# Optimization experiments

Hardware: AMD Instinct MI355X
Metric: run time of the kernel (lower is better)

## Reference

```python
import jax, jax.numpy as jnp
import numpy as np

N, T = 4096, 1024
COND, PRED, PERIOD = 896, 56, 7


def setup_inputs() -> dict:
    key = jax.random.key(0)
    k1, k2 = jax.random.split(key)
    query = jax.random.normal(k1, (N, T), dtype=jnp.float32)
    # learned per-location params: [init_level, level_sm_logit, init_trend,
    #  trend_sm_logit, season_sm, period seasonality logits]
    params = 0.1 * jax.random.normal(k2, (N, 5 + PERIOD), dtype=jnp.float32)
    return {"query": query, "params": params}


def _forward(query, params):
    init_level = params[:, 0]                       # [N]
    level_sm = jax.nn.sigmoid(params[:, 1])         # [N]
    init_trend = params[:, 2]                       # [N]
    trend_sm = jax.nn.sigmoid(params[:, 3])         # [N]
    season_sm = params[:, 4]                        # NOTE: no sigmoid, matches original code
    init_seas = jax.nn.sigmoid(params[:, -PERIOD:])  # [N, PERIOD]

    def step(carry, y):
        prev_level, prev_trend, buf = carry          # buf: rolling window of last PERIOD seasonalities
        s_t = buf[:, 0]                              # seasonalities[t]
        pred = prev_level + prev_trend
        level = level_sm * y + (1.0 - level_sm) * pred
        diff = jnp.abs(level - prev_level)
        trend = trend_sm * (level - prev_level) + (1.0 - trend_sm) * prev_trend
        new_seas = season_sm * (y - pred) + (1.0 - season_sm) * s_t
        buf = jnp.concatenate([buf[:, 1:], new_seas[:, None]], axis=1)
        return (level, trend, buf), (level, trend, new_seas, diff)

    carry0 = (init_level, init_trend, init_seas)
    _, (levels, trends, new_seas_seq, diffs) = jax.lax.scan(step, carry0, query.T)
    levels = levels.T            # [N, T]
    trends = trends.T            # [N, T]
    new_seas_seq = new_seas_seq.T  # [N, T], == seasonalities[:, PERIOD:]
    level_diffs = diffs.T.mean(axis=1)  # [N]

    # full seasonality sequence: PERIOD initial values followed by T computed ones
    seas_full = jnp.concatenate([init_seas, new_seas_seq], axis=1)  # [N, PERIOD+T]

    sm = query - levels - new_seas_seq  # [N, T]

    horizon = jnp.arange(1, PRED + 1, dtype=levels.dtype)  # [PRED]
    last_levels = levels[:, COND - 1:, None]   # [N, W, 1], W = T-COND+1
    last_trends = trends[:, COND - 1:, None]
    pr = last_levels + last_trends * horizon   # [N, W, PRED]

    # cyclic seasonality forecast per window
    season_index = jnp.tile(jnp.arange(PERIOD), (PRED + PERIOD - 1) // PERIOD)[:PRED]
    starts = jnp.arange(COND, T + 1)           # [W]
    idx = starts[:, None] + season_index[None, :]  # [W, PRED]
    pr = pr + seas_full[:, idx]                # [N, W, PRED]

    return sm, pr, level_diffs


def reference(query, params):
    return _forward(query, params)
```

## Files before the change

### kernel.cpp

```cpp
#include <hip/hip_runtime.h>
#include <cmath>

#define NROWS 4096
#define TLEN  1024
#define RPB   8
#define LT0   895
#define ST0   889
#define LTN   129
#define STN   135
#define PRV4R 1806
#define PRV4B (RPB * PRV4R)

__device__ __forceinline__ float sigmoidf_(float x) {
    return 1.0f / (1.0f + expf(-x));
}

__device__ __forceinline__ float f4c(const float4& v, int k) {
    switch (k & 3) { case 0: return v.x; case 1: return v.y; case 2: return v.z; default: return v.w; }
}

__global__ __launch_bounds__(256, 2)
void es_fused(const float* __restrict__ query,
              const float* __restrict__ params,
              float* __restrict__ sm,
              float* __restrict__ diffs,
              float4* __restrict__ pr4)
{
    __shared__ float lds_P[RPB * 65];
    __shared__ float lds_start[RPB * 65];
    __shared__ float lds_q[RPB * 225];
    __shared__ float lds_dsum[RPB * 33];
    __shared__ float lds_par[RPB * 16];
    __shared__ float Ltl[RPB * 132];
    __shared__ float Ttl[RPB * 132];
    __shared__ float Stl[RPB * 136];

    const int tid = threadIdx.x;
    const int r = tid >> 5;
    const int k = tid & 31;
    const int n = blockIdx.x * RPB + r;

    const float* pp = params + (size_t)n * 12;
    const float a  = sigmoidf_(pp[1]);
    const float b  = sigmoidf_(pp[3]);
    const float c  = pp[4];
    const float ia = 1.0f - a, ib = 1.0f - b, ic = 1.0f - c;

    float4 yv[8];
    {
        const float4* qv = reinterpret_cast<const float4*>(query + (size_t)n * TLEN + k * 32);
        #pragma unroll
        for (int i = 0; i < 8; ++i) yv[i] = qv[i];
    }

    {
        float L = 0.0f, B = 0.0f;
        #pragma unroll
        for (int j = 0; j < 32; ++j) {
            const float yy = f4c(yv[j >> 2], j);
            const float pred  = L + B;
            const float level = fmaf(a, yy, ia * pred);
            const float trend = fmaf(b, level - L, ib * B);
            L = level; B = trend;
        }
        lds_P[r * 65 + 2 * k]     = L;
        lds_P[r * 65 + 2 * k + 1] = B;
    }
    if (k == 0) {
        float* par = &lds_par[r * 16];
        par[0] = pp[0];
        par[1] = pp[2];
        par[2] = ia;
        par[3] = -(a * b);
        par[4] = ib + b * ia;
        par[5] = ic;
        #pragma unroll
        for (int l = 0; l < 7; ++l) par[6 + l] = sigmoidf_(pp[5 + l]);
    }
    __syncthreads();

    if (tid < 8) {
        const float* par = &lds_par[tid * 16];
        float m00 = par[2], m01 = par[2], m10 = par[3], m11 = par[4];
        #pragma unroll
        for (int s = 0; s < 5; ++s) {
            const float t00 = m00 * m00 + m01 * m10;
            const float t01 = m00 * m01 + m01 * m11;
            const float t10 = m10 * m00 + m11 * m10;
            const float t11 = m10 * m01 + m11 * m11;
            m00 = t00; m01 = t01; m10 = t10; m11 = t11;
        }
        float P0[32], P1[32];
        #pragma unroll
        for (int kk = 0; kk < 32; ++kk) {
            P0[kk] = lds_P[tid * 65 + 2 * kk];
            P1[kk] = lds_P[tid * 65 + 2 * kk + 1];
        }
        float s0 = par[0], s1 = par[1];
        #pragma unroll
        for (int kk = 0; kk < 32; ++kk) {
            lds_start[tid * 65 + 2 * kk]     = s0;
            lds_start[tid * 65 + 2 * kk + 1] = s1;
            const float t0 = m00 * s0 + m01 * s1 + P0[kk];
            const float t1 = m10 * s0 + m11 * s1 + P1[kk];
            s0 = t0; s1 = t1;
        }
    }
    __syncthreads();

    const float st0 = lds_start[r * 65 + 2 * k];
    const float st1 = lds_start[r * 65 + 2 * k + 1];

    {
        float L = st0, B = st1, dsum = 0.0f;
        float q[7] = {0,0,0,0,0,0,0};
        #pragma unroll
        for (int j = 0; j < 32; ++j) {
            const float yy = f4c(yv[j >> 2], j);
            const float pred  = L + B;
            const float level = fmaf(a, yy, ia * pred);
            const float d     = level - L;
            dsum += fabsf(d);
            const float trend = fmaf(b, d, ib * B);
            const float e     = yy - pred;
            q[j % 7] = fmaf(ic, q[j % 7], c * e);
            L = level; B = trend;
        }
        const int kp = (4 * k) % 7;
        #pragma unroll
        for (int l = 0; l < 7; ++l) {
            int g = kp + l; if (g >= 7) g -= 7;
            lds_q[r * 225 + k * 7 + g] = q[l];
        }
        lds_dsum[r * 33 + k] = dsum;
    }
    __syncthreads();

    if (tid < 56) {
        const int rr = tid / 7, p = tid % 7;
        const float icc = lds_par[rr * 16 + 5];
        const float ic2 = icc * icc;
        const float ic4 = ic2 * ic2;
        const float ic5 = ic4 * icc;
        float v = lds_par[rr * 16 + 6 + p];
        float qq[32];
        #pragma unroll
        for (int kk = 0; kk < 32; ++kk) qq[kk] = lds_q[rr * 225 + kk * 7 + p];
        int l = p;
        #pragma unroll
        for (int kk = 0; kk < 32; ++kk) {
            const float m = (l < 4) ? ic5 : ic4;
            const float nv = fmaf(m, v, qq[kk]);
            lds_q[rr * 225 + kk * 7 + p] = v;
            v = nv;
            l += 3; if (l >= 7) l -= 7;
        }
    } else if (tid < 64) {
        const int rr = tid - 56;
        float s = 0.0f;
        #pragma unroll
        for (int kk = 0; kk < 32; ++kk) s += lds_dsum[rr * 33 + kk];
        diffs[blockIdx.x * RPB + rr] = s * (1.0f / 1024.0f);
    }
    __syncthreads();

    {
        float sg[7];
        const int kp = (4 * k) % 7;
        #pragma unroll
        for (int l = 0; l < 7; ++l) {
            int g = kp + l; if (g >= 7) g -= 7;
            sg[l] = lds_q[r * 225 + k * 7 + g];
        }
        float L = st0, B = st1;
        float4 ov;
        float* smrow = sm + (size_t)n * TLEN + k * 32;
        #pragma unroll
        for (int j = 0; j < 32; ++j) {
            const float yy = f4c(yv[j >> 2], j);
            const float pred  = L + B;
            const float level = fmaf(a, yy, ia * pred);
            const float trend = fmaf(b, level - L, ib * B);
            const float e     = yy - pred;
            const float sn    = fmaf(ic, sg[j % 7], c * e);
            sg[j % 7] = sn;
            const float smv = (yy - level) - sn;
            switch (j & 3) { case 0: ov.x = smv; break; case 1: ov.y = smv; break;
                             case 2: ov.z = smv; break; default: ov.w = smv; }
            if ((j & 3) == 3) *reinterpret_cast<float4*>(smrow + (j - 3)) = ov;
            const int tg = k * 32 + j;
            if (tg >= ST0) Stl[r * 136 + tg - ST0] = sn;
            if (tg >= LT0) {
                Ltl[r * 132 + tg - LT0] = level;
                Ttl[r * 132 + tg - LT0] = trend;
            }
            L = level; B = trend;
        }
    }
    __syncthreads();

    {
        float4* prb = pr4 + (size_t)blockIdx.x * PRV4B;
        #pragma unroll 4
        for (int i = 0; i < 57; ++i) {
            const int q = i * 256 + tid;
            if (q < PRV4B) {
                const int row = q / PRV4R;
                const int rem = q - row * PRV4R;
                const int s   = rem / 14;
                const int h4  = rem - s * 14;
                const float L = Ltl[row * 132 + s];
                const float T = Ttl[row * 132 + s];
                const float* stp = &Stl[row * 136 + s];
                const int hb = h4 * 4;
                int m0 = hb % 7;
                int m1 = m0 + 1; if (m1 >= 7) m1 -= 7;
                int m2 = m0 + 2; if (m2 >= 7) m2 -= 7;
                int m3 = m0 + 3; if (m3 >= 7) m3 -= 7;
                float4 o;
                o.x = fmaf(T, (float)(hb + 1), L) + stp[m0];
                o.y = fmaf(T, (float)(hb + 2), L) + stp[m1];
                o.z = fmaf(T, (float)(hb + 3), L) + stp[m2];
                o.w = fmaf(T, (float)(hb + 4), L) + stp[m3];
                prb[q] = o;
            }
        }
    }
}

extern "C" void kernel_launch(void* const* d_in, const int* in_sizes, int n_in,
                              void* d_out, int out_size, void* d_ws, size_t ws_size,
                              hipStream_t stream) {
    const float* query  = (const float*)d_in[0];
    const float* params = (const float*)d_in[1];

    float* out   = (float*)d_out;
    float* sm    = out;
    float* pr    = out + (size_t)NROWS * TLEN;
    float* diffs = pr  + (size_t)NROWS * 129 * 56;

    hipLaunchKernelGGL(es_fused, dim3(NROWS / RPB), dim3(256), 0, stream,
                       query, params, sm, diffs, (float4*)pr);
}
```

Baseline: 36.16 us.

## Cache level and error per step, interleave sm stores with pr writeout

The second recurrence pass now saves per-step prediction errors and levels in registers, so the final pass no longer recomputes the level/trend recurrence. Only the lanes covering the tail window (k>=27) write sm and the LDS tiles before the barrier. All other lanes defer their sm computation and stores into the pr writeout loop, interleaving them with the pr float4 stores so both output streams share that phase. This adds 64 live floats per thread, which may raise register pressure and lower occupancy under launch_bounds(256,2).

After: 39.25 us. 8.6% more time.

```diff
diff --git a/kernel.cpp b/kernel.cpp
--- a/kernel.cpp
+++ b/kernel.cpp
@@ -111,6 +111,7 @@
     const float st0 = lds_start[r * 65 + 2 * k];
     const float st1 = lds_start[r * 65 + 2 * k + 1];
 
+    float e[32], lv[32];
     {
         float L = st0, B = st1, dsum = 0.0f;
         float q[7] = {0,0,0,0,0,0,0};
@@ -122,8 +123,10 @@
             const float d     = level - L;
             dsum += fabsf(d);
             const float trend = fmaf(b, d, ib * B);
-            const float e     = yy - pred;
-            q[j % 7] = fmaf(ic, q[j % 7], c * e);
+            const float ee    = yy - pred;
+            e[j]  = ee;
+            lv[j] = level;
+            q[j % 7] = fmaf(ic, q[j % 7], c * ee);
             L = level; B = trend;
         }
         const int kp = (4 * k) % 7;
@@ -164,47 +167,52 @@
     }
     __syncthreads();
 
-    {
-        float sg[7];
+    float sg[7];
+    {
         const int kp = (4 * k) % 7;
         #pragma unroll
         for (int l = 0; l < 7; ++l) {
             int g = kp + l; if (g >= 7) g -= 7;
             sg[l] = lds_q[r * 225 + k * 7 + g];
         }
-        float L = st0, B = st1;
+    }
+
+    if (k >= 27) {
+        float sgt[7];
+        #pragma unroll
+        for (int l = 0; l < 7; ++l) sgt[l] = sg[l];
+        float Bv = st1, prevL = st0;
         float4 ov;
         float* smrow = sm + (size_t)n * TLEN + k * 32;
         #pragma unroll
         for (int j = 0; j < 32; ++j) {
-            const float yy = f4c(yv[j >> 2], j);
-            const float pred  = L + B;
-            const float level = fmaf(a, yy, ia * pred);
-            const float trend = fmaf(b, level - L, ib * B);
-            const float e     = yy - pred;
-            const float sn    = fmaf(ic, sg[j % 7], c * e);
-            sg[j % 7] = sn;
-            const float smv = (yy - level) - sn;
+            const float sn = fmaf(ic, sgt[j % 7], c * e[j]);
+            sgt[j % 7] = sn;
+            const float d     = lv[j] - prevL;
+            const float trend = fmaf(b, d, ib * Bv);
+            Bv = trend; prevL = lv[j];
+            const float smv = (f4c(yv[j >> 2], j) - lv[j]) - sn;
             switch (j & 3) { case 0: ov.x = smv; break; case 1: ov.y = smv; break;
                              case 2: ov.z = smv; break; default: ov.w = smv; }
             if ((j & 3) == 3) *reinterpret_cast<float4*>(smrow + (j - 3)) = ov;
             const int tg = k * 32 + j;
             if (tg >= ST0) Stl[r * 136 + tg - ST0] = sn;
             if (tg >= LT0) {
-                Ltl[r * 132 + tg - LT0] = level;
+                Ltl[r * 132 + tg - LT0] = lv[j];
                 Ttl[r * 132 + tg - LT0] = trend;
             }
-            L = level; B = trend;
         }
     }
     __syncthreads();
 
     {
         float4* prb = pr4 + (size_t)blockIdx.x * PRV4B;
-        #pragma unroll 4
-        for (int i = 0; i < 57; ++i) {
-            const int q = i * 256 + tid;
-            if (q < PRV4B) {
+        float* smrow = sm + (size_t)n * TLEN + k * 32;
+        #pragma unroll
+        for (int blkq = 0; blkq < 8; ++blkq) {
+            #pragma unroll
+            for (int t = 0; t < 7; ++t) {
+                const int q = (blkq * 7 + t) * 256 + tid;
                 const int row = q / PRV4R;
                 const int rem = q - row * PRV4R;
                 const int s   = rem / 14;
@@ -224,6 +232,40 @@
                 o.w = fmaf(T, (float)(hb + 4), L) + stp[m3];
                 prb[q] = o;
             }
+            if (k < 27) {
+                float4 ov;
+                #pragma unroll
+                for (int u = 0; u < 4; ++u) {
+                    const int j = blkq * 4 + u;
+                    const float sn = fmaf(ic, sg[j % 7], c * e[j]);
+                    sg[j % 7] = sn;
+                    const float smv = (f4c(yv[j >> 2], j) - lv[j]) - sn;
+                    switch (u) { case 0: ov.x = smv; break; case 1: ov.y = smv; break;
+                                 case 2: ov.z = smv; break; default: ov.w = smv; }
+                }
+                *reinterpret_cast<float4*>(smrow + blkq * 4) = ov;
+            }
+        }
+        const int q = 56 * 256 + tid;
+        if (q < PRV4B) {
+            const int row = q / PRV4R;
+            const int rem = q - row * PRV4R;
+            const int s   = rem / 14;
+            const int h4  = rem - s * 14;
+            const float L = Ltl[row * 132 + s];
+            const float T = Ttl[row * 132 + s];
+            const float* stp = &Stl[row * 136 + s];
+            const int hb = h4 * 4;
+            int m0 = hb % 7;
+            int m1 = m0 + 1; if (m1 >= 7) m1 -= 7;
+            int m2 = m0 + 2; if (m2 >= 7) m2 -= 7;
+            int m3 = m0 + 3; if (m3 >= 7) m3 -= 7;
+            float4 o;
+            o.x = fmaf(T, (float)(hb + 1), L) + stp[m0];
+            o.y = fmaf(T, (float)(hb + 2), L) + stp[m1];
+            o.z = fmaf(T, (float)(hb + 3), L) + stp[m2];
+            o.w = fmaf(T, (float)(hb + 4), L) + stp[m3];
+            prb[q] = o;
         }
     }
 }
```
